# Optimization experiments

Measured on AMD Instinct MI355X. Metric: run time of the kernel, lower is better.

Reference implementation:

```python
import jax, jax.numpy as jnp
import numpy as np

D_MODEL = 1024
HEADS = 16
D_K = D_MODEL // HEADS
B, S = 2, 2048


def setup_inputs() -> dict:
    key = jax.random.key(0)
    ks = jax.random.split(key, 11)
    sc = 1.0 / np.sqrt(D_MODEL)
    inp = {
        "q": jax.random.normal(ks[0], (B, S, D_MODEL), jnp.float32),
        "k": jax.random.normal(ks[1], (B, S, D_MODEL), jnp.float32),
        "v": jax.random.normal(ks[2], (B, S, D_MODEL), jnp.float32),
        # causal mask, broadcastable to (B, H, S, S); 0 -> masked
        "mask": jnp.tril(jnp.ones((S, S), jnp.int32))[None, None],
        "w_q": jax.random.normal(ks[3], (D_MODEL, D_MODEL), jnp.float32) * sc,
        "b_q": jax.random.normal(ks[4], (D_MODEL,), jnp.float32) * sc,
        "w_k": jax.random.normal(ks[5], (D_MODEL, D_MODEL), jnp.float32) * sc,
        "b_k": jax.random.normal(ks[6], (D_MODEL,), jnp.float32) * sc,
        "w_v": jax.random.normal(ks[7], (D_MODEL, D_MODEL), jnp.float32) * sc,
        "b_v": jax.random.normal(ks[8], (D_MODEL,), jnp.float32) * sc,
        "w_o": jax.random.normal(ks[9], (D_MODEL, D_MODEL), jnp.float32) * sc,
        "b_o": jax.random.normal(ks[10], (D_MODEL,), jnp.float32) * sc,
    }
    return inp


def reference(q, k, v, mask, w_q, b_q, w_k, b_k, w_v, b_v, w_o, b_o):
    b = q.shape[0]
    # torch Linear: x @ W.T + b
    Q = q @ w_q.T + b_q
    K = k @ w_k.T + b_k
    V = v @ w_v.T + b_v
    # (B, S, D) -> (B, H, S, d_k)
    Q = Q.reshape(b, -1, HEADS, D_K).transpose(0, 2, 1, 3)
    K = K.reshape(b, -1, HEADS, D_K).transpose(0, 2, 1, 3)
    V = V.reshape(b, -1, HEADS, D_K).transpose(0, 2, 1, 3)
    scores = jnp.einsum("bhqd,bhkd->bhqk", Q, K) / np.sqrt(D_K).astype(np.float32)
    scores = jnp.where(mask == 0, -jnp.inf, scores)
    attn = jax.nn.softmax(scores, axis=-1)
    out = jnp.einsum("bhqk,bhkd->bhqd", attn, V)
    out = out.transpose(0, 2, 1, 3).reshape(b, -1, D_MODEL)
    # dropout is identity in eval mode
    return out @ w_o.T + b_o
```

## Files before the change

kernel.cpp:

```cpp
#include <hip/hip_runtime.h>
#include <math.h>

#define D_MODEL 1024
#define N_HEADS 16
#define DKH     64
#define BATCH   2
#define SEQ     2048
#define NT128   (SEQ/128)
#define PARTS_PER_BH 40

typedef unsigned short u16;
typedef unsigned long long u64;
typedef __attribute__((ext_vector_type(8))) short short8;
typedef __attribute__((ext_vector_type(4))) short s4v;
typedef __attribute__((ext_vector_type(4))) float f32x4;

__device__ __forceinline__ u16 f2bf(float f) {
    unsigned u = __float_as_uint(f);
    u += 0x7fffu + ((u >> 16) & 1u);
    return (u16)(u >> 16);
}
__device__ __forceinline__ float bf2f(u16 x) {
    return __int_as_float(((int)x) << 16);
}

__device__ __forceinline__ float fexp2(float x) {
#if __has_builtin(__builtin_amdgcn_exp2f)
    return __builtin_amdgcn_exp2f(x);
#else
    return exp2f(x);
#endif
}

__device__ __forceinline__ void gll16(const void* g, void* l) {
    __builtin_amdgcn_global_load_lds((const __attribute__((address_space(1))) void*)g,
                                     (__attribute__((address_space(3))) void*)l, 16, 0, 0);
}

__device__ __forceinline__ f32x4 mfma16(s4v a, s4v b, f32x4 c) {
#if __has_builtin(__builtin_amdgcn_mfma_f32_16x16x16bf16_1k)
    return __builtin_amdgcn_mfma_f32_16x16x16bf16_1k(a, b, c, 0, 0, 0);
#elif __has_builtin(__builtin_amdgcn_mfma_f32_16x16x16_bf16)
    return __builtin_amdgcn_mfma_f32_16x16x16_bf16(a, b, c, 0, 0, 0);
#else
    f32x4 d;
    asm("v_mfma_f32_16x16x16_bf16 %0, %1, %2, %3" : "=v"(d) : "v"(a), "v"(b), "v"(c));
    return d;
#endif
}

__device__ __forceinline__ int vperm(int d) {
    return ((d & 7) << 3) | (((d >> 3) & 1) << 2);
}

__global__ __launch_bounds__(256)
void convert_kernel(const float* __restrict__ q, const float* __restrict__ k,
                    const float* __restrict__ v, const float* __restrict__ wq,
                    const float* __restrict__ wk, const float* __restrict__ wv,
                    const float* __restrict__ wo,
                    u16* __restrict__ qb, u16* __restrict__ kb, u16* __restrict__ vb,
                    u16* __restrict__ wqb, u16* __restrict__ wkb,
                    u16* __restrict__ wvb, u16* __restrict__ wob)
{
    const size_t NV = ((size_t)16 << 20) >> 3;
    for (size_t i = (size_t)blockIdx.x * blockDim.x + threadIdx.x; i < NV;
         i += (size_t)gridDim.x * blockDim.x) {
        const size_t e = i << 3;
        const float* s; u16* d; size_t off;
        if (e < ((size_t)12 << 20)) {
            const int seg = (int)(e >> 22);
            off = e & (((size_t)1 << 22) - 1);
            s = seg == 0 ? q : seg == 1 ? k : v;
            d = seg == 0 ? qb : seg == 1 ? kb : vb;
        } else {
            const size_t r = e - ((size_t)12 << 20);
            const int seg = (int)(r >> 20);
            off = r & (((size_t)1 << 20) - 1);
            s = seg == 0 ? wq : seg == 1 ? wk : seg == 2 ? wv : wo;
            d = seg == 0 ? wqb : seg == 1 ? wkb : seg == 2 ? wvb : wob;
        }
        const float4 f0 = *(const float4*)(s + off);
        const float4 f1 = *(const float4*)(s + off + 4);
        short8 o;
        o[0]=(short)f2bf(f0.x); o[1]=(short)f2bf(f0.y); o[2]=(short)f2bf(f0.z); o[3]=(short)f2bf(f0.w);
        o[4]=(short)f2bf(f1.x); o[5]=(short)f2bf(f1.y); o[6]=(short)f2bf(f1.z); o[7]=(short)f2bf(f1.w);
        *(short8*)(d + off) = o;
    }
}

#define GEMM_PREAMBLE                                                            \
    __shared__ __align__(16) u16 As[2][128][32];                                 \
    __shared__ __align__(16) u16 Bs[2][128][32];                                 \
    const int tid  = threadIdx.x;                                                \
    const int lane = tid & 63;                                                   \
    const int wid  = tid >> 6;                                                   \
    const int wm   = wid >> 1, wn = wid & 1;                                     \
    const int lr   = lane & 15, lg = lane >> 4;                                  \
    const int mb   = blockIdx.x * 128, nb = blockIdx.y * 128;                    \
    const int g_row = lane >> 2;                                                 \
    const int g_col = (lane & 3) << 3;                                           \
    const u16* Ab = A  + (size_t)mb * K;                                         \
    const u16* Bb = Bw + (size_t)nb * K;                                         \
    f32x4 acc[4][4];                                                             \
    _Pragma("unroll")                                                            \
    for (int i = 0; i < 4; ++i)                                                  \
        _Pragma("unroll")                                                        \
        for (int j = 0; j < 4; ++j) { f32x4 z = {0.f,0.f,0.f,0.f}; acc[i][j] = z; }

#define STAGE(buf, kt)                                                           \
    {                                                                            \
        _Pragma("unroll")                                                        \
        for (int t = 0; t < 2; ++t) {                                            \
            const int r0 = t*64 + wid*16;                                        \
            gll16(&Ab[(size_t)(r0 + g_row)*K + (kt) + g_col], &As[buf][r0][0]);  \
            gll16(&Bb[(size_t)(r0 + g_row)*K + (kt) + g_col], &Bs[buf][r0][0]);  \
        }                                                                        \
    }

#define GEMM_MAINLOOP                                                            \
    STAGE(0, 0)                                                                  \
    __syncthreads();                                                             \
    const int NK = K >> 5;                                                       \
    for (int it = 0; it < NK; ++it) {                                            \
        const int c = it & 1;                                                    \
        if (it + 1 < NK) STAGE(c ^ 1, (it + 1) << 5)                             \
        short8 a[4], b[4];                                                       \
        _Pragma("unroll")                                                        \
        for (int i = 0; i < 4; ++i) a[i] = *(const short8*)&As[c][wm*64 + i*16 + lr][lg*8]; \
        _Pragma("unroll")                                                        \
        for (int j = 0; j < 4; ++j) b[j] = *(const short8*)&Bs[c][wn*64 + j*16 + lr][lg*8]; \
        _Pragma("unroll")                                                        \
        for (int i = 0; i < 4; ++i)                                              \
            _Pragma("unroll")                                                    \
            for (int j = 0; j < 4; ++j)                                          \
                acc[i][j] = __builtin_amdgcn_mfma_f32_16x16x32_bf16(a[i], b[j], acc[i][j], 0, 0, 0); \
        __syncthreads();                                                         \
    }

__global__ __launch_bounds__(256, 3)
void gemm_qkv_kernel(const u16* __restrict__ qb, const u16* __restrict__ kb,
                     const u16* __restrict__ vb, const u16* __restrict__ wqb,
                     const u16* __restrict__ wkb, const u16* __restrict__ wvb,
                     const float* __restrict__ b_q, const float* __restrict__ b_k,
                     const float* __restrict__ b_v,
                     u16* __restrict__ Qh, u16* __restrict__ Kh, u16* __restrict__ Vt,
                     int M, int N, int K)
{
    const int z = blockIdx.z;
    const u16* A    = z == 0 ? qb  : z == 1 ? kb  : vb;
    const u16* Bw   = z == 0 ? wqb : z == 1 ? wkb : wvb;
    const float* bias = z == 0 ? b_q : z == 1 ? b_k : b_v;
    u16* dst        = z == 0 ? Qh  : z == 1 ? Kh  : Vt;
    const float scale = z == 0 ? 0.18033688f : 1.0f;

    GEMM_PREAMBLE
    GEMM_MAINLOOP

    #pragma unroll
    for (int i = 0; i < 4; ++i) {
        #pragma unroll
        for (int j = 0; j < 4; ++j) {
            const int mbase = mb + wm*64 + i*16 + lg*4;
            const int n     = nb + wn*64 + j*16 + lr;
            const float bn  = bias[n];
            const int h = n >> 6, d = n & 63;
            #pragma unroll
            for (int r = 0; r < 4; ++r) {
                const int m = mbase + r;
                const int b = m >> 11, s = m & (SEQ - 1);
                const float val = (acc[i][j][r] + bn) * scale;
                if (z == 2) {
                    const int sp = (s & ~63) | ((s & 63) ^ vperm(d));
                    dst[(((size_t)(b*N_HEADS + h))*DKH + d)*SEQ + sp] = f2bf(val);
                } else {
                    dst[(((size_t)(b*N_HEADS + h))*SEQ + s)*DKH + d] = f2bf(val);
                }
            }
        }
    }
}

__global__ __launch_bounds__(256)
void gemm_out_kernel(const u16* __restrict__ A, const u16* __restrict__ Bw,
                     const float* __restrict__ bias, float* __restrict__ dst,
                     int M, int N, int K)
{
    __shared__ __align__(16) u16 As[2][128][32];
    __shared__ __align__(16) u16 Bs[2][64][32];

    const int tid  = threadIdx.x;
    const int lane = tid & 63;
    const int wid  = tid >> 6;
    const int wm   = wid >> 1, wn = wid & 1;
    const int lr   = lane & 15, lg = lane >> 4;
    const int mb   = blockIdx.x * 128, nb = blockIdx.y * 64;
    const int g_row = lane >> 2;
    const int g_col = (lane & 3) << 3;

    const u16* Ab = A  + (size_t)mb * K;
    const u16* Bb = Bw + (size_t)nb * K;

    f32x4 acc[4][2];
    #pragma unroll
    for (int i = 0; i < 4; ++i)
        #pragma unroll
        for (int j = 0; j < 2; ++j) { f32x4 z = {0.f,0.f,0.f,0.f}; acc[i][j] = z; }

#define OSTAGE(buf, kt)                                                          \
    {                                                                            \
        _Pragma("unroll")                                                        \
        for (int t = 0; t < 2; ++t) {                                            \
            const int r0 = t*64 + wid*16;                                        \
            gll16(&Ab[(size_t)(r0 + g_row)*K + (kt) + g_col], &As[buf][r0][0]);  \
        }                                                                        \
        gll16(&Bb[(size_t)(wid*16 + g_row)*K + (kt) + g_col], &Bs[buf][wid*16][0]); \
    }

    OSTAGE(0, 0)
    __syncthreads();

    const int NK = K >> 5;
    for (int it = 0; it < NK; ++it) {
        const int c = it & 1;
        if (it + 1 < NK) OSTAGE(c ^ 1, (it + 1) << 5)

        short8 a[4], b[2];
        #pragma unroll
        for (int i = 0; i < 4; ++i) a[i] = *(const short8*)&As[c][wm*64 + i*16 + lr][lg*8];
        #pragma unroll
        for (int j = 0; j < 2; ++j) b[j] = *(const short8*)&Bs[c][wn*32 + j*16 + lr][lg*8];
        #pragma unroll
        for (int i = 0; i < 4; ++i)
            #pragma unroll
            for (int j = 0; j < 2; ++j)
                acc[i][j] = __builtin_amdgcn_mfma_f32_16x16x32_bf16(a[i], b[j], acc[i][j], 0, 0, 0);

        __syncthreads();
    }
#undef OSTAGE

    #pragma unroll
    for (int i = 0; i < 4; ++i) {
        #pragma unroll
        for (int j = 0; j < 2; ++j) {
            const int mbase = mb + wm*64 + i*16 + lg*4;
            const int n     = nb + wn*32 + j*16 + lr;
            const float bn  = bias[n];
            #pragma unroll
            for (int r = 0; r < 4; ++r)
                dst[(size_t)(mbase + r) * N + n] = acc[i][j][r] + bn;
        }
    }
}

__device__ __forceinline__ void attn_step(
    const short8& aq0, const short8& aq1,
    f32x4 (&o)[4], float& osum, float& m_run,
    const u16 (*__restrict__ Kl)[64], const u16 (*__restrict__ Vl)[64],
    int kvb, int qbw, int lr, int lg)
{
    const int ksw  = (lr & 7) << 3;
    const int pvsw = vperm(lr);
    f32x4 st[4];
    __builtin_amdgcn_s_setprio(1);
    #pragma unroll
    for (int c = 0; c < 4; ++c) {
        const int kr = c*16 + lr;
        f32x4 z = {0.f,0.f,0.f,0.f};
        short8 k0 = *(const short8*)&Kl[kr][( 0 + lg*8) ^ ksw];
        short8 k1 = *(const short8*)&Kl[kr][(32 + lg*8) ^ ksw];
        z = __builtin_amdgcn_mfma_f32_16x16x32_bf16(k0, aq0, z, 0, 0, 0);
        z = __builtin_amdgcn_mfma_f32_16x16x32_bf16(k1, aq1, z, 0, 0, 0);
        st[c] = z;
    }
    __builtin_amdgcn_s_setprio(0);

    if (kvb + 63 > qbw) {
        #pragma unroll
        for (int c = 0; c < 4; ++c)
            #pragma unroll
            for (int r = 0; r < 4; ++r)
                if (kvb + c*16 + lg*4 + r > qbw + lr) st[c][r] = -INFINITY;
    }

    float tm = fmaxf(fmaxf(st[0][0], st[0][1]), fmaxf(st[0][2], st[0][3]));
    #pragma unroll
    for (int c = 1; c < 4; ++c)
        tm = fmaxf(tm, fmaxf(fmaxf(st[c][0], st[c][1]), fmaxf(st[c][2], st[c][3])));
    tm = fmaxf(tm, __shfl_xor(tm, 16));
    tm = fmaxf(tm, __shfl_xor(tm, 32));

    if (__any(tm > m_run + 11.5f)) {
        const float mnew  = fmaxf(m_run, tm);
        const float alpha = fexp2(m_run - mnew);
        m_run = mnew;
        osum *= alpha;
        float af[4];
        #pragma unroll
        for (int r = 0; r < 4; ++r)
            af[r] = __shfl(alpha, (lg << 4) | (lg*4 + r));
        #pragma unroll
        for (int db = 0; db < 4; ++db)
            #pragma unroll
            for (int r = 0; r < 4; ++r) o[db][r] *= af[r];
    }

    s4v av[4];
    float sum = 0.f;
    #pragma unroll
    for (int c = 0; c < 4; ++c) {
        const float p0 = fexp2(st[c][0] - m_run);
        const float p1 = fexp2(st[c][1] - m_run);
        const float p2 = fexp2(st[c][2] - m_run);
        const float p3 = fexp2(st[c][3] - m_run);
        sum += (p0 + p1) + (p2 + p3);
        unsigned lo, hi;
        asm("v_cvt_pk_bf16_f32 %0, %1, %2" : "=v"(lo) : "v"(p0), "v"(p1));
        asm("v_cvt_pk_bf16_f32 %0, %1, %2" : "=v"(hi) : "v"(p2), "v"(p3));
        union { unsigned u[2]; s4v s; } uu;
        uu.u[0] = lo; uu.u[1] = hi;
        av[c] = uu.s;
    }
    osum += sum;

    __builtin_amdgcn_s_setprio(1);
    #pragma unroll
    for (int c = 0; c < 4; ++c) {
        #pragma unroll
        for (int db = 0; db < 4; ++db) {
            union { u64 q; s4v s; } bv;
            bv.q = *(const u64*)&Vl[db*16 + lr][(c*16 + lg*4) ^ pvsw];
            o[db] = mfma16(av[c], bv.s, o[db]);
        }
    }
    __builtin_amdgcn_s_setprio(0);
}

__global__ __launch_bounds__(512)
void flash_split_kernel(const u16* __restrict__ Qh, const u16* __restrict__ Kh,
                        const u16* __restrict__ Vt, u16* __restrict__ part_o,
                        float* __restrict__ part_ms)
{
    __shared__ __align__(16) u16 Kl[2][64][64];
    __shared__ __align__(16) u16 Vl[2][64][64];

    const int x = 39 - blockIdx.x;
    int t, ch;
    if      (x <  4) { t = x;                 ch = 0;        }
    else if (x < 12) { t = 4 + ((x-4) >> 1);  ch = (x-4)&1;  }
    else if (x < 24) { t = 8 + (x-12)/3;      ch = (x-12)%3; }
    else             { t = 12 + ((x-24) >> 2); ch = (x-24)&3; }

    const int tid  = threadIdx.x;
    const int lane = tid & 63;
    const int wid  = tid >> 6;
    const int lr   = lane & 15, lg = lane >> 4;
    const int bh   = blockIdx.y;
    const int qbw  = t*128 + wid*16;
    const size_t base = (size_t)bh * SEQ * DKH;

    const int c0      = ch * 8;
    const int nc_here = min(8, 2*(t+1) - c0);

    const int srow8 = lane >> 3;
    const int srow  = wid*8 + srow8;
    const int kcol  = ((lane & 7) << 3) ^ (srow8 << 3);
    const int vcol  = (lane & 7) << 3;

#define FSTAGE(buf, kb)                                                          \
    {                                                                            \
        gll16(&Kh[base + (size_t)((kb) + srow)*DKH + kcol], &Kl[buf][wid*8][0]); \
        gll16(&Vt[base + (size_t)srow*SEQ + (kb) + vcol],  &Vl[buf][wid*8][0]);  \
    }

    short8 aq0 = *(const short8*)&Qh[base + (size_t)(qbw + lr)*DKH +  0 + lg*8];
    short8 aq1 = *(const short8*)&Qh[base + (size_t)(qbw + lr)*DKH + 32 + lg*8];

    f32x4 o[4];
    float osum = 0.f, m_run = -INFINITY;
    {
        f32x4 z = {0.f,0.f,0.f,0.f};
        #pragma unroll
        for (int db = 0; db < 4; ++db) o[db] = z;
    }

    FSTAGE(0, c0*64)
    __syncthreads();

    for (int ci = 0; ci < nc_here; ++ci) {
        const int p = ci & 1;
        if (ci + 1 < nc_here) FSTAGE(p ^ 1, (c0 + ci + 1)*64)

        const int kvb = (c0 + ci) * 64;
        if (kvb <= qbw + 15)
            attn_step(aq0, aq1, o, osum, m_run, Kl[p], Vl[p], kvb, qbw, lr, lg);

        __syncthreads();
    }
#undef FSTAGE

    osum += __shfl_xor(osum, 16);
    osum += __shfl_xor(osum, 32);

    const size_t slot = (size_t)bh * PARTS_PER_BH + x;
    u16*   po = part_o  + (slot << 13);
    float* pm = part_ms + (slot << 8);
    #pragma unroll
    for (int db = 0; db < 4; ++db)
        #pragma unroll
        for (int r = 0; r < 4; ++r)
            po[(wid*16 + lg*4 + r)*64 + db*16 + lr] = f2bf(o[db][r]);
    if (lane < 16) {
        pm[(wid*16 + lane)*2 + 0] = m_run;
        pm[(wid*16 + lane)*2 + 1] = osum;
    }
}

__global__ __launch_bounds__(256)
void merge_kernel(const u16* __restrict__ part_o, const float* __restrict__ part_ms,
                  u16* __restrict__ attb)
{
    const int t   = blockIdx.x;
    const int bh  = blockIdx.y;
    const int nch = min(4, (2*(t+1) + 7) >> 3);
    const int basex = t < 4 ? t : t < 8 ? 4 + 2*(t-4) : t < 12 ? 12 + 3*(t-8) : 24 + 4*(t-12);

    const int row = threadIdx.x >> 1;
    const int cb  = (threadIdx.x & 1) * 32;

    float mm[4], ss[4];
    float M = -INFINITY;
    for (int c = 0; c < nch; ++c) {
        const size_t slot = (size_t)bh * PARTS_PER_BH + basex + c;
        mm[c] = part_ms[(slot << 8) + row*2 + 0];
        ss[c] = part_ms[(slot << 8) + row*2 + 1];
        M = fmaxf(M, mm[c]);
    }
    float S = 0.f;
    float acc[32];
    #pragma unroll
    for (int j = 0; j < 32; ++j) acc[j] = 0.f;
    for (int c = 0; c < nch; ++c) {
        const float w = exp2f(mm[c] - M);
        S += w * ss[c];
        const size_t slot = (size_t)bh * PARTS_PER_BH + basex + c;
        const u16* po = part_o + (slot << 13) + row*64 + cb;
        #pragma unroll
        for (int g = 0; g < 4; ++g) {
            short8 v = *(const short8*)(po + g*8);
            #pragma unroll
            for (int j = 0; j < 8; ++j)
                acc[g*8 + j] += w * bf2f((u16)v[j]);
        }
    }
    const float inv = 1.f / S;
    const int b = bh >> 4, h = bh & 15;
    const int grow = t*128 + row;
    u16* dst = attb + ((size_t)(b*SEQ + grow))*D_MODEL + h*64 + cb;
    #pragma unroll
    for (int g = 0; g < 4; ++g) {
        short8 ov;
        #pragma unroll
        for (int j = 0; j < 8; ++j) ov[j] = (short)f2bf(acc[g*8 + j] * inv);
        *(short8*)(dst + g*8) = ov;
    }
}

extern "C" void kernel_launch(void* const* d_in, const int* in_sizes, int n_in,
                              void* d_out, int out_size, void* d_ws, size_t ws_size,
                              hipStream_t stream)
{
    const float* q   = (const float*)d_in[0];
    const float* k   = (const float*)d_in[1];
    const float* v   = (const float*)d_in[2];
    const float* w_q = (const float*)d_in[4];
    const float* b_q = (const float*)d_in[5];
    const float* w_k = (const float*)d_in[6];
    const float* b_k = (const float*)d_in[7];
    const float* w_v = (const float*)d_in[8];
    const float* b_v = (const float*)d_in[9];
    const float* w_o = (const float*)d_in[10];
    const float* b_o = (const float*)d_in[11];

    char* ws = (char*)d_ws;
    const size_t MB = 1024*1024;
    u16* Qh   = (u16*)(ws +  0*MB);
    u16* Kh   = (u16*)(ws +  8*MB);
    u16* Vt   = (u16*)(ws + 16*MB);
    u16* qb   = (u16*)(ws + 24*MB);
    u16* kb   = (u16*)(ws + 32*MB);
    u16* vb   = (u16*)(ws + 40*MB);
    u16* wqb  = (u16*)(ws + 48*MB);
    u16* wkb  = (u16*)(ws + 50*MB);
    u16* wvb  = (u16*)(ws + 52*MB);
    u16* wob  = (u16*)(ws + 54*MB);
    u16* attb = qb;
    u16*   part_o  = (u16*)(ws + 32*MB);
    float* part_ms = (float*)(ws + 52*MB);

    const int M = BATCH * SEQ, N = D_MODEL, K = D_MODEL;

    convert_kernel<<<2048, 256, 0, stream>>>(q, k, v, w_q, w_k, w_v, w_o,
                                             qb, kb, vb, wqb, wkb, wvb, wob);
    gemm_qkv_kernel<<<dim3(M/128, N/128, 3), 256, 0, stream>>>(
        qb, kb, vb, wqb, wkb, wvb, b_q, b_k, b_v, Qh, Kh, Vt, M, N, K);
    flash_split_kernel<<<dim3(PARTS_PER_BH, BATCH*N_HEADS), 512, 0, stream>>>(
        Qh, Kh, Vt, part_o, part_ms);
    merge_kernel<<<dim3(NT128, BATCH*N_HEADS), 256, 0, stream>>>(part_o, part_ms, attb);
    gemm_out_kernel<<<dim3(M/128, N/64), 256, 0, stream>>>(attb, wob, b_o, (float*)d_out, M, N, K);
}
```

Baseline: 131.2 us.

## Process two 16-row query tiles per wave to reuse K/V fragments

Each wave in the flash attention kernel now handles 32 query rows as two 16-row sub-tiles, so a block covers 256 queries. Every K and V fragment read from shared memory feeds two MFMAs, which halves LDS traffic and K/V staging per query. The split grid shrinks from 40 to 20 parts per head, and the merge kernel is rewritten for 256-row tiles. The cost is more registers per wave and fewer blocks in flight, which lowers parallelism and occupancy.

```diff
diff --git a/kernel.cpp b/kernel.cpp
--- a/kernel.cpp
+++ b/kernel.cpp
@@ -6,8 +6,8 @@
 #define DKH     64
 #define BATCH   2
 #define SEQ     2048
-#define NT128   (SEQ/128)
-#define PARTS_PER_BH 40
+#define NT256   (SEQ/256)
+#define PARTS_PER_BH 20
 
 typedef unsigned short u16;
 typedef unsigned long long u64;
@@ -253,48 +253,60 @@
     }
 }
 
-__device__ __forceinline__ void attn_step(
-    const short8& aq0, const short8& aq1,
-    f32x4 (&o)[4], float& osum, float& m_run,
+__device__ __forceinline__ void attn_step2(
+    const short8& aq00, const short8& aq01,
+    const short8& aq10, const short8& aq11,
+    f32x4 (&o0)[4], f32x4 (&o1)[4],
+    float& osum0, float& osum1, float& m0, float& m1,
     const u16 (*__restrict__ Kl)[64], const u16 (*__restrict__ Vl)[64],
-    int kvb, int qbw, int lr, int lg)
+    int kvb, int qbw0, int qbw1, int lr, int lg)
 {
     const int ksw  = (lr & 7) << 3;
     const int pvsw = vperm(lr);
-    f32x4 st[4];
+    f32x4 st0[4], st1[4];
     __builtin_amdgcn_s_setprio(1);
     #pragma unroll
     for (int c = 0; c < 4; ++c) {
         const int kr = c*16 + lr;
-        f32x4 z = {0.f,0.f,0.f,0.f};
         short8 k0 = *(const short8*)&Kl[kr][( 0 + lg*8) ^ ksw];
         short8 k1 = *(const short8*)&Kl[kr][(32 + lg*8) ^ ksw];
-        z = __builtin_amdgcn_mfma_f32_16x16x32_bf16(k0, aq0, z, 0, 0, 0);
-        z = __builtin_amdgcn_mfma_f32_16x16x32_bf16(k1, aq1, z, 0, 0, 0);
-        st[c] = z;
+        f32x4 z0 = {0.f,0.f,0.f,0.f}, z1 = {0.f,0.f,0.f,0.f};
+        z0 = __builtin_amdgcn_mfma_f32_16x16x32_bf16(k0, aq00, z0, 0, 0, 0);
+        z1 = __builtin_amdgcn_mfma_f32_16x16x32_bf16(k0, aq10, z1, 0, 0, 0);
+        z0 = __builtin_amdgcn_mfma_f32_16x16x32_bf16(k1, aq01, z0, 0, 0, 0);
+        z1 = __builtin_amdgcn_mfma_f32_16x16x32_bf16(k1, aq11, z1, 0, 0, 0);
+        st0[c] = z0; st1[c] = z1;
     }
     __builtin_amdgcn_s_setprio(0);
 
-    if (kvb + 63 > qbw) {
+    if (kvb + 63 > qbw0) {
         #pragma unroll
         for (int c = 0; c < 4; ++c)
             #pragma unroll
             for (int r = 0; r < 4; ++r)
-                if (kvb + c*16 + lg*4 + r > qbw + lr) st[c][r] = -INFINITY;
-    }
-
-    float tm = fmaxf(fmaxf(st[0][0], st[0][1]), fmaxf(st[0][2], st[0][3]));
-    #pragma unroll
-    for (int c = 1; c < 4; ++c)
-        tm = fmaxf(tm, fmaxf(fmaxf(st[c][0], st[c][1]), fmaxf(st[c][2], st[c][3])));
-    tm = fmaxf(tm, __shfl_xor(tm, 16));
-    tm = fmaxf(tm, __shfl_xor(tm, 32));
-
-    if (__any(tm > m_run + 11.5f)) {
-        const float mnew  = fmaxf(m_run, tm);
-        const float alpha = fexp2(m_run - mnew);
-        m_run = mnew;
-        osum *= alpha;
+                if (kvb + c*16 + lg*4 + r > qbw0 + lr) st0[c][r] = -INFINITY;
+    }
+    if (kvb + 63 > qbw1) {
+        #pragma unroll
+        for (int c = 0; c < 4; ++c)
+            #pragma unroll
+            for (int r = 0; r < 4; ++r)
+                if (kvb + c*16 + lg*4 + r > qbw1 + lr) st1[c][r] = -INFINITY;
+    }
+
+    float tl0 = fmaxf(fmaxf(st0[0][0], st0[0][1]), fmaxf(st0[0][2], st0[0][3]));
+    float tl1 = fmaxf(fmaxf(st1[0][0], st1[0][1]), fmaxf(st1[0][2], st1[0][3]));
+    #pragma unroll
+    for (int c = 1; c < 4; ++c) {
+        tl0 = fmaxf(tl0, fmaxf(fmaxf(st0[c][0], st0[c][1]), fmaxf(st0[c][2], st0[c][3])));
+        tl1 = fmaxf(tl1, fmaxf(fmaxf(st1[c][0], st1[c][1]), fmaxf(st1[c][2], st1[c][3])));
+    }
+    if (__any(tl0 > m0 + 11.5f)) {
+        float tm = fmaxf(tl0, __shfl_xor(tl0, 16));
+        tm = fmaxf(tm, __shfl_xor(tm, 32));
+        const float mnew  = fmaxf(m0, tm);
+        const float alpha = fexp2(m0 - mnew);
+        m0 = mnew; osum0 *= alpha;
         float af[4];
         #pragma unroll
         for (int r = 0; r < 4; ++r)
@@ -302,26 +314,53 @@
         #pragma unroll
         for (int db = 0; db < 4; ++db)
             #pragma unroll
-            for (int r = 0; r < 4; ++r) o[db][r] *= af[r];
-    }
-
-    s4v av[4];
-    float sum = 0.f;
+            for (int r = 0; r < 4; ++r) o0[db][r] *= af[r];
+    }
+    if (__any(tl1 > m1 + 11.5f)) {
+        float tm = fmaxf(tl1, __shfl_xor(tl1, 16));
+        tm = fmaxf(tm, __shfl_xor(tm, 32));
+        const float mnew  = fmaxf(m1, tm);
+        const float alpha = fexp2(m1 - mnew);
+        m1 = mnew; osum1 *= alpha;
+        float af[4];
+        #pragma unroll
+        for (int r = 0; r < 4; ++r)
+            af[r] = __shfl(alpha, (lg << 4) | (lg*4 + r));
+        #pragma unroll
+        for (int db = 0; db < 4; ++db)
+            #pragma unroll
+            for (int r = 0; r < 4; ++r) o1[db][r] *= af[r];
+    }
+
+    s4v av0[4], av1[4];
+    float sum0 = 0.f, sum1 = 0.f;
     #pragma unroll
     for (int c = 0; c < 4; ++c) {
-        const float p0 = fexp2(st[c][0] - m_run);
-        const float p1 = fexp2(st[c][1] - m_run);
-        const float p2 = fexp2(st[c][2] - m_run);
-        const float p3 = fexp2(st[c][3] - m_run);
-        sum += (p0 + p1) + (p2 + p3);
+        const float p0 = fexp2(st0[c][0] - m0);
+        const float p1 = fexp2(st0[c][1] - m0);
+        const float p2 = fexp2(st0[c][2] - m0);
+        const float p3 = fexp2(st0[c][3] - m0);
+        sum0 += (p0 + p1) + (p2 + p3);
         unsigned lo, hi;
         asm("v_cvt_pk_bf16_f32 %0, %1, %2" : "=v"(lo) : "v"(p0), "v"(p1));
         asm("v_cvt_pk_bf16_f32 %0, %1, %2" : "=v"(hi) : "v"(p2), "v"(p3));
-        union { unsigned u[2]; s4v s; } uu;
-        uu.u[0] = lo; uu.u[1] = hi;
-        av[c] = uu.s;
-    }
-    osum += sum;
+        union { unsigned u[2]; s4v s; } uu; uu.u[0] = lo; uu.u[1] = hi;
+        av0[c] = uu.s;
+    }
+    #pragma unroll
+    for (int c = 0; c < 4; ++c) {
+        const float p0 = fexp2(st1[c][0] - m1);
+        const float p1 = fexp2(st1[c][1] - m1);
+        const float p2 = fexp2(st1[c][2] - m1);
+        const float p3 = fexp2(st1[c][3] - m1);
+        sum1 += (p0 + p1) + (p2 + p3);
+        unsigned lo, hi;
+        asm("v_cvt_pk_bf16_f32 %0, %1, %2" : "=v"(lo) : "v"(p0), "v"(p1));
+        asm("v_cvt_pk_bf16_f32 %0, %1, %2" : "=v"(hi) : "v"(p2), "v"(p3));
+        union { unsigned u[2]; s4v s; } uu; uu.u[0] = lo; uu.u[1] = hi;
+        av1[c] = uu.s;
+    }
+    osum0 += sum0; osum1 += sum1;
 
     __builtin_amdgcn_s_setprio(1);
     #pragma unroll
@@ -330,7 +369,8 @@
         for (int db = 0; db < 4; ++db) {
             union { u64 q; s4v s; } bv;
             bv.q = *(const u64*)&Vl[db*16 + lr][(c*16 + lg*4) ^ pvsw];
-            o[db] = mfma16(av[c], bv.s, o[db]);
+            o0[db] = mfma16(av0[c], bv.s, o0[db]);
+            o1[db] = mfma16(av1[c], bv.s, o1[db]);
         }
     }
     __builtin_amdgcn_s_setprio(0);
@@ -344,23 +384,28 @@
     __shared__ __align__(16) u16 Kl[2][64][64];
     __shared__ __align__(16) u16 Vl[2][64][64];
 
-    const int x = 39 - blockIdx.x;
-    int t, ch;
-    if      (x <  4) { t = x;                 ch = 0;        }
-    else if (x < 12) { t = 4 + ((x-4) >> 1);  ch = (x-4)&1;  }
-    else if (x < 24) { t = 8 + (x-12)/3;      ch = (x-12)%3; }
-    else             { t = 12 + ((x-24) >> 2); ch = (x-24)&3; }
+    const int x = 19 - blockIdx.x;
+    int t2, ch;
+    if      (x <  1) { t2 = 0; ch = 0;      }
+    else if (x <  2) { t2 = 1; ch = 0;      }
+    else if (x <  4) { t2 = 2; ch = x - 2;  }
+    else if (x <  6) { t2 = 3; ch = x - 4;  }
+    else if (x <  9) { t2 = 4; ch = x - 6;  }
+    else if (x < 12) { t2 = 5; ch = x - 9;  }
+    else if (x < 16) { t2 = 6; ch = x - 12; }
+    else             { t2 = 7; ch = x - 16; }
 
     const int tid  = threadIdx.x;
     const int lane = tid & 63;
     const int wid  = tid >> 6;
     const int lr   = lane & 15, lg = lane >> 4;
     const int bh   = blockIdx.y;
-    const int qbw  = t*128 + wid*16;
+    const int qbw0 = t2*256 + wid*32;
+    const int qbw1 = qbw0 + 16;
     const size_t base = (size_t)bh * SEQ * DKH;
 
     const int c0      = ch * 8;
-    const int nc_here = min(8, 2*(t+1) - c0);
+    const int nc_here = min(8, 4*(t2+1) - c0);
 
     const int srow8 = lane >> 3;
     const int srow  = wid*8 + srow8;
@@ -373,15 +418,17 @@
         gll16(&Vt[base + (size_t)srow*SEQ + (kb) + vcol],  &Vl[buf][wid*8][0]);  \
     }
 
-    short8 aq0 = *(const short8*)&Qh[base + (size_t)(qbw + lr)*DKH +  0 + lg*8];
-    short8 aq1 = *(const short8*)&Qh[base + (size_t)(qbw + lr)*DKH + 32 + lg*8];
-
-    f32x4 o[4];
-    float osum = 0.f, m_run = -INFINITY;
+    short8 aq00 = *(const short8*)&Qh[base + (size_t)(qbw0 + lr)*DKH +  0 + lg*8];
+    short8 aq01 = *(const short8*)&Qh[base + (size_t)(qbw0 + lr)*DKH + 32 + lg*8];
+    short8 aq10 = *(const short8*)&Qh[base + (size_t)(qbw1 + lr)*DKH +  0 + lg*8];
+    short8 aq11 = *(const short8*)&Qh[base + (size_t)(qbw1 + lr)*DKH + 32 + lg*8];
+
+    f32x4 o0[4], o1[4];
+    float osum0 = 0.f, osum1 = 0.f, m0 = -INFINITY, m1 = -INFINITY;
     {
         f32x4 z = {0.f,0.f,0.f,0.f};
         #pragma unroll
-        for (int db = 0; db < 4; ++db) o[db] = z;
+        for (int db = 0; db < 4; ++db) { o0[db] = z; o1[db] = z; }
     }
 
     FSTAGE(0, c0*64)
@@ -392,38 +439,46 @@
         if (ci + 1 < nc_here) FSTAGE(p ^ 1, (c0 + ci + 1)*64)
 
         const int kvb = (c0 + ci) * 64;
-        if (kvb <= qbw + 15)
-            attn_step(aq0, aq1, o, osum, m_run, Kl[p], Vl[p], kvb, qbw, lr, lg);
+        if (kvb <= qbw1 + 15)
+            attn_step2(aq00, aq01, aq10, aq11, o0, o1, osum0, osum1, m0, m1,
+                       Kl[p], Vl[p], kvb, qbw0, qbw1, lr, lg);
 
         __syncthreads();
     }
 #undef FSTAGE
 
-    osum += __shfl_xor(osum, 16);
-    osum += __shfl_xor(osum, 32);
+    osum0 += __shfl_xor(osum0, 16);
+    osum0 += __shfl_xor(osum0, 32);
+    osum1 += __shfl_xor(osum1, 16);
+    osum1 += __shfl_xor(osum1, 32);
 
     const size_t slot = (size_t)bh * PARTS_PER_BH + x;
-    u16*   po = part_o  + (slot << 13);
-    float* pm = part_ms + (slot << 8);
+    u16*   po = part_o  + (slot << 14);
+    float* pm = part_ms + (slot << 9);
     #pragma unroll
     for (int db = 0; db < 4; ++db)
         #pragma unroll
-        for (int r = 0; r < 4; ++r)
-            po[(wid*16 + lg*4 + r)*64 + db*16 + lr] = f2bf(o[db][r]);
+        for (int r = 0; r < 4; ++r) {
+            po[(wid*32      + lg*4 + r)*64 + db*16 + lr] = f2bf(o0[db][r]);
+            po[(wid*32 + 16 + lg*4 + r)*64 + db*16 + lr] = f2bf(o1[db][r]);
+        }
     if (lane < 16) {
-        pm[(wid*16 + lane)*2 + 0] = m_run;
-        pm[(wid*16 + lane)*2 + 1] = osum;
-    }
-}
-
-__global__ __launch_bounds__(256)
+        pm[(wid*32      + lane)*2 + 0] = m0;
+        pm[(wid*32      + lane)*2 + 1] = osum0;
+        pm[(wid*32 + 16 + lane)*2 + 0] = m1;
+        pm[(wid*32 + 16 + lane)*2 + 1] = osum1;
+    }
+}
+
+__global__ __launch_bounds__(512)
 void merge_kernel(const u16* __restrict__ part_o, const float* __restrict__ part_ms,
                   u16* __restrict__ attb)
 {
-    const int t   = blockIdx.x;
+    const int t2  = blockIdx.x;
     const int bh  = blockIdx.y;
-    const int nch = min(4, (2*(t+1) + 7) >> 3);
-    const int basex = t < 4 ? t : t < 8 ? 4 + 2*(t-4) : t < 12 ? 12 + 3*(t-8) : 24 + 4*(t-12);
+    const int nch = (t2 >> 1) + 1;
+    const int bxt[8] = {0, 1, 2, 4, 6, 9, 12, 16};
+    const int basex = bxt[t2];
 
     const int row = threadIdx.x >> 1;
     const int cb  = (threadIdx.x & 1) * 32;
@@ -432,8 +487,8 @@
     float M = -INFINITY;
     for (int c = 0; c < nch; ++c) {
         const size_t slot = (size_t)bh * PARTS_PER_BH + basex + c;
-        mm[c] = part_ms[(slot << 8) + row*2 + 0];
-        ss[c] = part_ms[(slot << 8) + row*2 + 1];
+        mm[c] = part_ms[(slot << 9) + row*2 + 0];
+        ss[c] = part_ms[(slot << 9) + row*2 + 1];
         M = fmaxf(M, mm[c]);
     }
     float S = 0.f;
@@ -444,7 +499,7 @@
         const float w = exp2f(mm[c] - M);
         S += w * ss[c];
         const size_t slot = (size_t)bh * PARTS_PER_BH + basex + c;
-        const u16* po = part_o + (slot << 13) + row*64 + cb;
+        const u16* po = part_o + (slot << 14) + row*64 + cb;
         #pragma unroll
         for (int g = 0; g < 4; ++g) {
             short8 v = *(const short8*)(po + g*8);
@@ -455,7 +510,7 @@
     }
     const float inv = 1.f / S;
     const int b = bh >> 4, h = bh & 15;
-    const int grow = t*128 + row;
+    const int grow = t2*256 + row;
     u16* dst = attb + ((size_t)(b*SEQ + grow))*D_MODEL + h*64 + cb;
     #pragma unroll
     for (int g = 0; g < 4; ++g) {
@@ -506,6 +561,6 @@
         qb, kb, vb, wqb, wkb, wvb, b_q, b_k, b_v, Qh, Kh, Vt, M, N, K);
     flash_split_kernel<<<dim3(PARTS_PER_BH, BATCH*N_HEADS), 512, 0, stream>>>(
         Qh, Kh, Vt, part_o, part_ms);
-    merge_kernel<<<dim3(NT128, BATCH*N_HEADS), 256, 0, stream>>>(part_o, part_ms, attb);
+    merge_kernel<<<dim3(NT256, BATCH*N_HEADS), 512, 0, stream>>>(part_o, part_ms, attb);
     gemm_out_kernel<<<dim3(M/128, N/64), 256, 0, stream>>>(attb, wob, b_o, (float*)d_out, M, N, K);
 }
```

Result: slower. 143.3 us (+9.2%).
